# Performance work log

Hardware: AMD Instinct MI355X
Metric: run time of the kernel (lower is better)

## Reference

```python
import jax, jax.numpy as jnp
import numpy as np

B, N, D, H = 8, 2048, 256, 4
HD = D // H


def setup_inputs() -> dict:
    key = jax.random.key(0)
    ks = jax.random.split(key, 12)
    s = 1.0 / np.sqrt(D)
    inp = {
        "node_features": jax.random.normal(ks[0], (B, N, D), dtype=jnp.float32),
        "causal_mask": jnp.tril(jnp.ones((N, N), dtype=jnp.float32)),
        "Wq": jax.random.normal(ks[1], (D, D), dtype=jnp.float32) * s,
        "bq": jnp.zeros((D,), dtype=jnp.float32),
        "Wk": jax.random.normal(ks[2], (D, D), dtype=jnp.float32) * s,
        "bk": jnp.zeros((D,), dtype=jnp.float32),
        "Wv": jax.random.normal(ks[3], (D, D), dtype=jnp.float32) * s,
        "bv": jnp.zeros((D,), dtype=jnp.float32),
        "Wo": jax.random.normal(ks[4], (D, D), dtype=jnp.float32) * s,
        "bo": jnp.zeros((D,), dtype=jnp.float32),
        "Wu": jax.random.normal(ks[5], (2 * D, D), dtype=jnp.float32) * (1.0 / np.sqrt(2 * D)),
        "bu": jnp.zeros((D,), dtype=jnp.float32),
    }
    return inp


def reference(node_features, causal_mask, Wq, bq, Wk, bk, Wv, bv, Wo, bo, Wu, bu):
    # node_features: [B, N, D]; causal_mask: [N, N] (1 = keep, 0 = masked)
    x = node_features
    # project and split heads -> [B, H, N, HD]
    def heads(w, b):
        return (x @ w + b).reshape(B, N, H, HD).transpose(0, 2, 1, 3)
    q, k, v = heads(Wq, bq), heads(Wk, bk), heads(Wv, bv)
    scale = 1.0 / np.sqrt(HD).astype(np.float32)
    scores = jnp.einsum("bhnd,bhmd->bhnm", q, k) * scale  # [B, H, N, N]
    scores = jnp.where(causal_mask > 0, scores, jnp.float32(-1e9))
    attn = jax.nn.softmax(scores, axis=-1)
    ctx = jnp.einsum("bhnm,bhmd->bhnd", attn, v)  # [B, H, N, HD]
    messages = ctx.transpose(0, 2, 1, 3).reshape(B, N, D) @ Wo + bo  # [B, N, D]
    combined = jnp.concatenate([x, messages], axis=-1)  # [B, N, 2D]
    updated = jax.nn.relu(combined @ Wu + bu)  # [B, N, D]  (dropout = identity in eval)
    return updated
```

## Files before the change

kernel.cpp:

```cpp
#include <hip/hip_runtime.h>
#include <math.h>

constexpr int B  = 8;
constexpr int N  = 2048;
constexpr int D  = 256;
constexpr int H  = 4;
constexpr int HD = 64;
constexpr int MTOT = B * N;

typedef __attribute__((ext_vector_type(8))) short  short8;
typedef __attribute__((ext_vector_type(4))) float  floatx4;
typedef unsigned short ushort_t;

#define QSCALE 0.1803368801111204f

__device__ __forceinline__ unsigned short f2bf(float f) {
    unsigned u = __float_as_uint(f);
    u += 0x7fffu + ((u >> 16) & 1u);
    return (unsigned short)(u >> 16);
}

__device__ __forceinline__ unsigned short f2bf_t(float f) {
    return (unsigned short)(__float_as_uint(f) >> 16);
}

__device__ __forceinline__ void gl_lds16(const ushort_t* g, ushort_t* l) {
    __builtin_amdgcn_global_load_lds(
        (const __attribute__((address_space(1))) void*)g,
        (__attribute__((address_space(3))) void*)l, 16, 0, 0);
}

__global__ __launch_bounds__(256) void prep(
    const float* __restrict__ x,
    const float* __restrict__ Wq, const float* __restrict__ Wk,
    const float* __restrict__ Wv, const float* __restrict__ Wo,
    const float* __restrict__ Wu,
    ushort_t* __restrict__ xb,
    ushort_t* __restrict__ wqkvt, ushort_t* __restrict__ wut,
    ushort_t* __restrict__ wbt,   ushort_t* __restrict__ wob)
{
    __shared__ float Ls[64][65];
    const int bx = blockIdx.x;
    const int t  = threadIdx.x;

    if (bx < 2048) {
        int idx = (bx * 256 + t) * 8;
        float4 a = *(const float4*)(x + idx);
        float4 b = *(const float4*)(x + idx + 4);
        ushort_t o[8] = {f2bf(a.x), f2bf(a.y), f2bf(a.z), f2bf(a.w),
                         f2bf(b.x), f2bf(b.y), f2bf(b.z), f2bf(b.w)};
        *(short8*)(xb + idx) = *(const short8*)o;
        return;
    }

    if (bx < 2112) {
        const int e  = bx - 2048;
        const int zz = e >> 4;
        const int kt = (e >> 2) & 3;
        const int nt = e & 3;
        const float* src; ushort_t* dst; int K;
        if      (zz == 0) { src = Wq; dst = wqkvt;          K = 256; }
        else if (zz == 1) { src = Wk; dst = wqkvt + 65536;  K = 256; }
        else if (zz == 2) { src = Wv; dst = wqkvt + 131072; K = 256; }
        else              { src = Wu; dst = wut;            K = 512; }
        #pragma unroll
        for (int i = 0; i < 16; i++) {
            int ee = t + i * 256, r = ee >> 6, c = ee & 63;
            Ls[r][c] = src[(size_t)(kt * 64 + r) * 256 + nt * 64 + c];
        }
        __syncthreads();
        #pragma unroll
        for (int i = 0; i < 16; i++) {
            int ee = t + i * 256, r = ee >> 6, c = ee & 63;
            dst[(size_t)(nt * 64 + r) * K + kt * 64 + c] = f2bf(Ls[c][r]);
        }
        return;
    }

    if (bx < 2128) {
        const int e  = bx - 2112;
        const int kt = e >> 2;
        const int nt = e & 3;
        #pragma unroll
        for (int i = 0; i < 16; i++) {
            int ee = t + i * 256, r = ee >> 6, c = ee & 63;
            Ls[r][c] = Wu[(size_t)(256 + kt * 64 + r) * 256 + nt * 64 + c];
        }
        __syncthreads();
        #pragma unroll
        for (int i = 0; i < 16; i++) {
            int ee = t + i * 256, r = ee >> 6, c = ee & 63;
            wbt[(size_t)(nt * 64 + r) * 256 + kt * 64 + c] = f2bf(Ls[c][r]);
        }
        return;
    }

    {
        int idx = ((bx - 2128) * 256 + t) * 8;
        float4 a = *(const float4*)(Wo + idx);
        float4 b = *(const float4*)(Wo + idx + 4);
        ushort_t o[8] = {f2bf(a.x), f2bf(a.y), f2bf(a.z), f2bf(a.w),
                         f2bf(b.x), f2bf(b.y), f2bf(b.z), f2bf(b.w)};
        *(short8*)(wob + idx) = *(const short8*)o;
    }
}

__global__ __launch_bounds__(256) void qkv_gemm(
    const ushort_t* __restrict__ xb, const ushort_t* __restrict__ wqkvt,
    const ushort_t* __restrict__ wob, const ushort_t* __restrict__ wbt,
    const float* __restrict__ Wu,
    const float* __restrict__ bq, const float* __restrict__ bk,
    const float* __restrict__ bv, const float* __restrict__ bo,
    const float* __restrict__ bu,
    ushort_t* __restrict__ q, ushort_t* __restrict__ kout,
    ushort_t* __restrict__ vt,
    ushort_t* __restrict__ wut, float* __restrict__ b2)
{
    __shared__ ushort_t SH[16896];
    ushort_t* As = SH;
    ushort_t* Bs = SH + 8192;

    const int t = threadIdx.x, w = t >> 6, lane = t & 63;
    const int quad = lane >> 4, l16 = lane & 15;
    const int bx = blockIdx.x;
    const int wr = (w >> 1) * 64, wc = (w & 1) * 64;

    if (blockIdx.y == 128) {
        if (bx < 4) {
            const int row0 = (bx >> 1) * 128;
            const int col0 = (bx & 1) * 128;
            floatx4 acc[4][4] = {};
            for (int k0 = 0; k0 < 256; k0 += 64) {
                __syncthreads();
                #pragma unroll
                for (int i = 0; i < 4; i++) {
                    int e = t + (i << 8);
                    int r = e >> 3, c8 = (e & 7) << 3;
                    gl_lds16(wob + (size_t)(row0 + r) * 256 + k0 + c8, &As[e * 8]);
                    gl_lds16(wbt + (size_t)(col0 + r) * 256 + k0 + c8, &Bs[e * 8]);
                }
                __syncthreads();
                #pragma unroll
                for (int kk = 0; kk < 64; kk += 32) {
                    short8 af[4], bf[4];
                    #pragma unroll
                    for (int i = 0; i < 4; i++)
                        af[i] = *(const short8*)&As[(wr + i * 16 + l16) * 64 + kk + quad * 8];
                    #pragma unroll
                    for (int j = 0; j < 4; j++)
                        bf[j] = *(const short8*)&Bs[(wc + j * 16 + l16) * 64 + kk + quad * 8];
                    #pragma unroll
                    for (int i = 0; i < 4; i++)
                        #pragma unroll
                        for (int j = 0; j < 4; j++)
                            acc[i][j] = __builtin_amdgcn_mfma_f32_16x16x32_bf16(
                                af[i], bf[j], acc[i][j], 0, 0, 0);
                }
            }
            #pragma unroll
            for (int j = 0; j < 4; j++) {
                int cl = wc + j * 16 + l16;
                #pragma unroll
                for (int i = 0; i < 4; i++)
                    #pragma unroll
                    for (int r = 0; r < 4; r++) {
                        int ml = wr + i * 16 + quad * 4 + r;
                        wut[(size_t)(col0 + cl) * 512 + 256 + row0 + ml] =
                            f2bf(acc[i][j][r]);
                    }
            }
        } else if (bx == 4) {
            float s0 = 0.f, s1 = 0.f, s2 = 0.f, s3 = 0.f;
            for (int j = 0; j < 64; j++) {
                s0 = fmaf(bo[j],       Wu[(size_t)(256 + j)       * 256 + t], s0);
                s1 = fmaf(bo[j + 64],  Wu[(size_t)(256 + j + 64)  * 256 + t], s1);
                s2 = fmaf(bo[j + 128], Wu[(size_t)(256 + j + 128) * 256 + t], s2);
                s3 = fmaf(bo[j + 192], Wu[(size_t)(256 + j + 192) * 256 + t], s3);
            }
            b2[t] = bu[t] + ((s0 + s1) + (s2 + s3));
        }
        return;
    }

    const int col0 = bx * 128, row0 = blockIdx.y * 128;

    floatx4 acc[4][4] = {};

    for (int k0 = 0; k0 < 256; k0 += 64) {
        __syncthreads();
        #pragma unroll
        for (int i = 0; i < 4; i++) {
            int e = t + (i << 8);
            int r = e >> 3, c8 = (e & 7) << 3;
            gl_lds16(xb    + (size_t)(row0 + r) * 256 + k0 + c8, &As[e * 8]);
            gl_lds16(wqkvt + (size_t)(col0 + r) * 256 + k0 + c8, &Bs[e * 8]);
        }
        __syncthreads();

        #pragma unroll
        for (int kk = 0; kk < 64; kk += 32) {
            short8 af[4], bf[4];
            #pragma unroll
            for (int i = 0; i < 4; i++)
                af[i] = *(const short8*)&As[(wr + i * 16 + l16) * 64 + kk + quad * 8];
            #pragma unroll
            for (int j = 0; j < 4; j++)
                bf[j] = *(const short8*)&Bs[(wc + j * 16 + l16) * 64 + kk + quad * 8];
            #pragma unroll
            for (int i = 0; i < 4; i++)
                #pragma unroll
                for (int j = 0; j < 4; j++)
                    acc[i][j] = __builtin_amdgcn_mfma_f32_16x16x32_bf16(
                        af[i], bf[j], acc[i][j], 0, 0, 0);
        }
    }

    const int kind = bx >> 1;
    const float* bias = (kind == 0) ? bq : (kind == 1 ? bk : bv);
    const float scl  = (kind == 0) ? QSCALE : 1.0f;
    __syncthreads();
    ushort_t (*Ts)[132] = (ushort_t(*)[132])SH;
    #pragma unroll
    for (int j = 0; j < 4; j++) {
        int cl = wc + j * 16 + l16;
        float bsv = bias[(bx & 1) * 128 + cl];
        #pragma unroll
        for (int i = 0; i < 4; i++) {
            #pragma unroll
            for (int r = 0; r < 4; r++) {
                int ml = wr + i * 16 + quad * 4 + r;
                ushort_t bvv = f2bf((acc[i][j][r] + bsv) * scl);
                if (kind < 2) Ts[ml][cl] = bvv;
                else          Ts[cl][ml] = bvv;
            }
        }
    }
    __syncthreads();

    const int b = row0 >> 11, n0 = row0 & (N - 1);
    #pragma unroll
    for (int i = 0; i < 8; i++) {
        int id = t + (i << 8);
        int rr = id >> 4, c8 = (id & 15) << 3;
        short8 val = *(const short8*)&Ts[rr][c8];
        if (kind < 2) {
            int cg = (bx & 1) * 128 + c8;
            int h = cg >> 6, hd = cg & 63;
            if (kind == 0) {
                *(short8*)&q[(((size_t)(b * H + h)) * N + n0 + rr) * HD + hd] = val;
            } else {
                int hd2 = (((hd >> 3) ^ (rr & 7)) << 3);
                *(short8*)&kout[(((size_t)(b * H + h)) * N + n0 + rr) * HD + hd2] = val;
            }
        } else {
            int cg = (bx & 1) * 128 + rr;
            int h = cg >> 6, hd = cg & 63;
            int u  = id & 15;
            int up = (u & 8) | ((u ^ hd) & 7);
            *(short8*)&vt[(((size_t)(b * H + h)) * HD + hd) * N + n0 + (up << 3)] = val;
        }
    }
}

__global__ __launch_bounds__(512) void attn_mfma(
    const ushort_t* __restrict__ q,
    const ushort_t* __restrict__ k,
    const ushort_t* __restrict__ vt,
    ushort_t* __restrict__ ctxb)
{
    __shared__ ushort_t Ks [128 * 64];
    __shared__ ushort_t Vts[64 * 128];
    __shared__ ushort_t Ps [8][16][36];

    const int t    = threadIdx.x;
    const int w    = t >> 6;
    const int lane = t & 63;
    const int quad = lane >> 4;
    const int l16  = lane & 15;
    const int swz  = l16 & 7;
    const int bh   = blockIdx.x;
    const int b    = bh >> 2, h = bh & 3;
    const int by   = blockIdx.y;
    const int grp  = w >> 2;
    const int qt   = grp ? by : (31 - by);
    const int qbase = qt * 64;
    const int rowb  = qbase + (w & 3) * 16;

    const ushort_t* qp = q  + (size_t)bh * N * HD;
    const ushort_t* kp = k  + (size_t)bh * N * HD;
    const ushort_t* vp = vt + (size_t)bh * HD * N;

    short8 qf0, qf1;
    {
        const ushort_t* qrow = qp + (size_t)(rowb + l16) * HD + quad * 8;
        qf0 = *(const short8*)(qrow);
        qf1 = *(const short8*)(qrow + 32);
    }

    floatx4 acc_o[4] = {};
    float plsum[4] = {};

    const int nkt_self = (qt >> 1) + 1;
    const int nkt_max  = ((31 - by) >> 1) + 1;

    for (int kt = 0; kt < nkt_max; kt++) {
        const int kbase = kt * 128;
        __syncthreads();

        #pragma unroll
        for (int i = 0; i < 2; i++) {
            int e = t + (i << 9);
            gl_lds16(kp + (((size_t)(kbase + (e >> 3))) << 6) + ((e & 7) << 3),
                     &Ks[e * 8]);
            gl_lds16(vp + (size_t)(e >> 4) * N + kbase + ((e & 15) << 3),
                     &Vts[e * 8]);
        }
        __syncthreads();

        if (kt >= nkt_self) continue;

        int rem = rowb + 15 - kbase;
        int nch = (rem < 0) ? 0 : ((rem >> 5) + 1);
        if (nch > 4) nch = 4;

        for (int ch = 0; ch < nch; ch++) {
            #pragma unroll
            for (int c2 = 0; c2 < 2; c2++) {
                const int ct = ch * 2 + c2;
                const int krow = (ct * 16 + l16) * 64;
                short8 kf0 = *(const short8*)&Ks[krow + ((quad ^ swz) << 3)];
                short8 kf1 = *(const short8*)&Ks[krow + (((4 + quad) ^ swz) << 3)];
                floatx4 z = {0.0f, 0.0f, 0.0f, 0.0f};
                floatx4 s = __builtin_amdgcn_mfma_f32_16x16x32_bf16(qf0, kf0, z, 0, 0, 0);
                s         = __builtin_amdgcn_mfma_f32_16x16x32_bf16(qf1, kf1, s, 0, 0, 0);
                const bool partial = (kbase + ct * 16 + 15) > rowb;
                if (partial) {
                    const int keyg = kbase + ct * 16 + l16;
                    #pragma unroll
                    for (int r = 0; r < 4; r++) {
                        float sv = s[r];
                        if (keyg > rowb + quad * 4 + r) sv = -3.0e38f;
                        float pv = __builtin_amdgcn_exp2f(sv);
                        plsum[r] += pv;
                        Ps[w][quad * 4 + r][c2 * 16 + l16] = f2bf_t(pv);
                    }
                } else {
                    #pragma unroll
                    for (int r = 0; r < 4; r++) {
                        float pv = __builtin_amdgcn_exp2f(s[r]);
                        plsum[r] += pv;
                        Ps[w][quad * 4 + r][c2 * 16 + l16] = f2bf_t(pv);
                    }
                }
            }
            short8 pf = *(const short8*)&Ps[w][l16][quad * 8];
            const int uu = ch * 4 + quad;
            const int up = (uu & 8) | ((uu ^ l16) & 7);
            #pragma unroll
            for (int nt = 0; nt < 4; nt++) {
                short8 vf = *(const short8*)&Vts[(nt * 16 + l16) * 128 + (up << 3)];
                acc_o[nt] = __builtin_amdgcn_mfma_f32_16x16x32_bf16(pf, vf, acc_o[nt], 0, 0, 0);
            }
        }
    }

    #pragma unroll
    for (int r = 0; r < 4; r++) {
        float l = plsum[r];
        l += __shfl_xor(l, 1);
        l += __shfl_xor(l, 2);
        l += __shfl_xor(l, 4);
        l += __shfl_xor(l, 8);
        float inv = 1.0f / l;
        int   n   = rowb + quad * 4 + r;
        #pragma unroll
        for (int nt = 0; nt < 4; nt++) {
            ctxb[((size_t)(b * N + n)) * D + h * HD + nt * 16 + l16] =
                f2bf(acc_o[nt][r] * inv);
        }
    }
}

__global__ __launch_bounds__(256) void tail2(
    const ushort_t* __restrict__ xb, const ushort_t* __restrict__ ctxb,
    const ushort_t* __restrict__ wut, const float* __restrict__ b2,
    float* __restrict__ out)
{
    __shared__ ushort_t As[64 * 64];
    __shared__ ushort_t Bs[128 * 64];

    const int t = threadIdx.x, w = t >> 6, lane = t & 63;
    const int quad = lane >> 4, l16 = lane & 15;
    const int col0 = blockIdx.x * 128, row0 = blockIdx.y * 64;
    const int wr = (w >> 1) * 32, wc = (w & 1) * 64;

    floatx4 acc[2][4] = {};

    for (int k0 = 0; k0 < 512; k0 += 64) {
        const ushort_t* Ab = (k0 < 256) ? xb : ctxb;
        const int ka = k0 & 255;
        __syncthreads();
        #pragma unroll
        for (int i = 0; i < 2; i++) {
            int e = t + (i << 8);
            int r = e >> 3, c8 = (e & 7) << 3;
            gl_lds16(Ab + (size_t)(row0 + r) * 256 + ka + c8, &As[e * 8]);
        }
        #pragma unroll
        for (int i = 0; i < 4; i++) {
            int e = t + (i << 8);
            int r = e >> 3, c8 = (e & 7) << 3;
            gl_lds16(wut + (size_t)(col0 + r) * 512 + k0 + c8, &Bs[e * 8]);
        }
        __syncthreads();

        #pragma unroll
        for (int kk = 0; kk < 64; kk += 32) {
            short8 af[2], bf[4];
            #pragma unroll
            for (int i = 0; i < 2; i++)
                af[i] = *(const short8*)&As[(wr + i * 16 + l16) * 64 + kk + quad * 8];
            #pragma unroll
            for (int j = 0; j < 4; j++)
                bf[j] = *(const short8*)&Bs[(wc + j * 16 + l16) * 64 + kk + quad * 8];
            #pragma unroll
            for (int i = 0; i < 2; i++)
                #pragma unroll
                for (int j = 0; j < 4; j++)
                    acc[i][j] = __builtin_amdgcn_mfma_f32_16x16x32_bf16(
                        af[i], bf[j], acc[i][j], 0, 0, 0);
        }
    }

    #pragma unroll
    for (int j = 0; j < 4; j++) {
        int col = col0 + wc + j * 16 + l16;
        float bsv = b2[col];
        #pragma unroll
        for (int i = 0; i < 2; i++) {
            #pragma unroll
            for (int r = 0; r < 4; r++) {
                int m = row0 + wr + i * 16 + quad * 4 + r;
                out[(size_t)m * 256 + col] = fmaxf(acc[i][j][r] + bsv, 0.0f);
            }
        }
    }
}

extern "C" void kernel_launch(void* const* d_in, const int* in_sizes, int n_in,
                              void* d_out, int out_size, void* d_ws, size_t ws_size,
                              hipStream_t stream)
{
    const float* x  = (const float*)d_in[0];
    const float* Wq = (const float*)d_in[2];
    const float* bq = (const float*)d_in[3];
    const float* Wk = (const float*)d_in[4];
    const float* bk = (const float*)d_in[5];
    const float* Wv = (const float*)d_in[6];
    const float* bv = (const float*)d_in[7];
    const float* Wo = (const float*)d_in[8];
    const float* bo = (const float*)d_in[9];
    const float* Wu = (const float*)d_in[10];
    const float* bu = (const float*)d_in[11];
    float* out = (float*)d_out;

    const size_t SZ = (size_t)MTOT * D;
    ushort_t* xb    = (ushort_t*)d_ws;
    ushort_t* qb    = xb    + SZ;
    ushort_t* kb    = qb    + SZ;
    ushort_t* vbt   = kb    + SZ;
    ushort_t* ctxb  = vbt   + SZ;
    ushort_t* wqkvt = ctxb  + SZ;
    ushort_t* wut   = wqkvt + 196608;
    ushort_t* wbt   = wut   + 131072;
    ushort_t* wob   = wbt   + 65536;
    float*    b2    = (float*)(wob + 65536);

    prep<<<2160, 256, 0, stream>>>(x, Wq, Wk, Wv, Wo, Wu,
                                   xb, wqkvt, wut, wbt, wob);

    qkv_gemm<<<dim3(6, 129), 256, 0, stream>>>(
        xb, wqkvt, wob, wbt, Wu, bq, bk, bv, bo, bu,
        qb, kb, vbt, wut, b2);

    attn_mfma<<<dim3(32, 16), 512, 0, stream>>>(qb, kb, vbt, ctxb);

    tail2<<<dim3(2, 256), 256, 0, stream>>>(xb, ctxb, wut, b2, out);
}
```

Measured before the change: 171.6 us.

## Double-buffer LDS tiles in QKV and tail GEMMs to overlap loads with MFMA

Both the QKV projection GEMM and the tail output GEMM now prefetch the next K-slice into a second LDS buffer while MFMAs run on the current one, replacing the load-sync-compute-sync loop with a single barrier per step. The QKV kernel shrinks its K-step to 32 so two buffers fit in the existing shared array, and it folds the W2 side-GEMM path into the same pipelined loop. The goal is to hide global-to-LDS latency. In exchange the tail kernel doubles its LDS footprint, which may reduce occupancy, and the QKV loop now has more iterations.

```diff
diff --git a/kernel.cpp b/kernel.cpp
--- a/kernel.cpp
+++ b/kernel.cpp
@@ -117,59 +117,15 @@
     ushort_t* __restrict__ wut, float* __restrict__ b2)
 {
     __shared__ ushort_t SH[16896];
-    ushort_t* As = SH;
-    ushort_t* Bs = SH + 8192;
 
     const int t = threadIdx.x, w = t >> 6, lane = t & 63;
     const int quad = lane >> 4, l16 = lane & 15;
     const int bx = blockIdx.x;
     const int wr = (w >> 1) * 64, wc = (w & 1) * 64;
-
-    if (blockIdx.y == 128) {
-        if (bx < 4) {
-            const int row0 = (bx >> 1) * 128;
-            const int col0 = (bx & 1) * 128;
-            floatx4 acc[4][4] = {};
-            for (int k0 = 0; k0 < 256; k0 += 64) {
-                __syncthreads();
-                #pragma unroll
-                for (int i = 0; i < 4; i++) {
-                    int e = t + (i << 8);
-                    int r = e >> 3, c8 = (e & 7) << 3;
-                    gl_lds16(wob + (size_t)(row0 + r) * 256 + k0 + c8, &As[e * 8]);
-                    gl_lds16(wbt + (size_t)(col0 + r) * 256 + k0 + c8, &Bs[e * 8]);
-                }
-                __syncthreads();
-                #pragma unroll
-                for (int kk = 0; kk < 64; kk += 32) {
-                    short8 af[4], bf[4];
-                    #pragma unroll
-                    for (int i = 0; i < 4; i++)
-                        af[i] = *(const short8*)&As[(wr + i * 16 + l16) * 64 + kk + quad * 8];
-                    #pragma unroll
-                    for (int j = 0; j < 4; j++)
-                        bf[j] = *(const short8*)&Bs[(wc + j * 16 + l16) * 64 + kk + quad * 8];
-                    #pragma unroll
-                    for (int i = 0; i < 4; i++)
-                        #pragma unroll
-                        for (int j = 0; j < 4; j++)
-                            acc[i][j] = __builtin_amdgcn_mfma_f32_16x16x32_bf16(
-                                af[i], bf[j], acc[i][j], 0, 0, 0);
-                }
-            }
-            #pragma unroll
-            for (int j = 0; j < 4; j++) {
-                int cl = wc + j * 16 + l16;
-                #pragma unroll
-                for (int i = 0; i < 4; i++)
-                    #pragma unroll
-                    for (int r = 0; r < 4; r++) {
-                        int ml = wr + i * 16 + quad * 4 + r;
-                        wut[(size_t)(col0 + cl) * 512 + 256 + row0 + ml] =
-                            f2bf(acc[i][j][r]);
-                    }
-            }
-        } else if (bx == 4) {
+    const bool isW2 = (blockIdx.y == 128);
+
+    if (isW2 && bx >= 4) {
+        if (bx == 4) {
             float s0 = 0.f, s1 = 0.f, s2 = 0.f, s3 = 0.f;
             for (int j = 0; j < 64; j++) {
                 s0 = fmaf(bo[j],       Wu[(size_t)(256 + j)       * 256 + t], s0);
@@ -182,43 +138,74 @@
         return;
     }
 
-    const int col0 = bx * 128, row0 = blockIdx.y * 128;
+    const int row0 = isW2 ? ((bx >> 1) * 128) : ((int)blockIdx.y * 128);
+    const int col0 = isW2 ? ((bx & 1) * 128) : (bx * 128);
+    const ushort_t* Ag = (isW2 ? wob : xb)    + (size_t)row0 * 256;
+    const ushort_t* Bg = (isW2 ? wbt : wqkvt) + (size_t)col0 * 256;
 
     floatx4 acc[4][4] = {};
 
-    for (int k0 = 0; k0 < 256; k0 += 64) {
-        __syncthreads();
-        #pragma unroll
-        for (int i = 0; i < 4; i++) {
+    {
+        #pragma unroll
+        for (int i = 0; i < 2; i++) {
             int e = t + (i << 8);
-            int r = e >> 3, c8 = (e & 7) << 3;
-            gl_lds16(xb    + (size_t)(row0 + r) * 256 + k0 + c8, &As[e * 8]);
-            gl_lds16(wqkvt + (size_t)(col0 + r) * 256 + k0 + c8, &Bs[e * 8]);
-        }
-        __syncthreads();
-
-        #pragma unroll
-        for (int kk = 0; kk < 64; kk += 32) {
-            short8 af[4], bf[4];
-            #pragma unroll
-            for (int i = 0; i < 4; i++)
-                af[i] = *(const short8*)&As[(wr + i * 16 + l16) * 64 + kk + quad * 8];
+            int r = e >> 2, c8 = (e & 3) << 3;
+            gl_lds16(Ag + (size_t)r * 256 + c8, SH + e * 8);
+            gl_lds16(Bg + (size_t)r * 256 + c8, SH + 8192 + e * 8);
+        }
+    }
+    __syncthreads();
+
+    for (int k = 0; k < 8; k++) {
+        const int buf = k & 1;
+        if (k < 7) {
+            const int nb = buf ^ 1;
+            const int k0 = (k + 1) * 32;
+            #pragma unroll
+            for (int i = 0; i < 2; i++) {
+                int e = t + (i << 8);
+                int r = e >> 2, c8 = (e & 3) << 3;
+                gl_lds16(Ag + (size_t)r * 256 + k0 + c8, SH + nb * 4096 + e * 8);
+                gl_lds16(Bg + (size_t)r * 256 + k0 + c8, SH + 8192 + nb * 4096 + e * 8);
+            }
+        }
+        const ushort_t* Al = SH + buf * 4096;
+        const ushort_t* Bl = SH + 8192 + buf * 4096;
+        short8 af[4], bf[4];
+        #pragma unroll
+        for (int i = 0; i < 4; i++)
+            af[i] = *(const short8*)&Al[(wr + i * 16 + l16) * 32 + quad * 8];
+        #pragma unroll
+        for (int j = 0; j < 4; j++)
+            bf[j] = *(const short8*)&Bl[(wc + j * 16 + l16) * 32 + quad * 8];
+        #pragma unroll
+        for (int i = 0; i < 4; i++)
             #pragma unroll
             for (int j = 0; j < 4; j++)
-                bf[j] = *(const short8*)&Bs[(wc + j * 16 + l16) * 64 + kk + quad * 8];
+                acc[i][j] = __builtin_amdgcn_mfma_f32_16x16x32_bf16(
+                    af[i], bf[j], acc[i][j], 0, 0, 0);
+        __syncthreads();
+    }
+
+    if (isW2) {
+        #pragma unroll
+        for (int j = 0; j < 4; j++) {
+            int cl = wc + j * 16 + l16;
             #pragma unroll
             for (int i = 0; i < 4; i++)
                 #pragma unroll
-                for (int j = 0; j < 4; j++)
-                    acc[i][j] = __builtin_amdgcn_mfma_f32_16x16x32_bf16(
-                        af[i], bf[j], acc[i][j], 0, 0, 0);
-        }
+                for (int r = 0; r < 4; r++) {
+                    int ml = wr + i * 16 + quad * 4 + r;
+                    wut[(size_t)(col0 + cl) * 512 + 256 + row0 + ml] =
+                        f2bf(acc[i][j][r]);
+                }
+        }
+        return;
     }
 
     const int kind = bx >> 1;
     const float* bias = (kind == 0) ? bq : (kind == 1 ? bk : bv);
     const float scl  = (kind == 0) ? QSCALE : 1.0f;
-    __syncthreads();
     ushort_t (*Ts)[132] = (ushort_t(*)[132])SH;
     #pragma unroll
     for (int j = 0; j < 4; j++) {
@@ -386,8 +373,8 @@
     const ushort_t* __restrict__ wut, const float* __restrict__ b2,
     float* __restrict__ out)
 {
-    __shared__ ushort_t As[64 * 64];
-    __shared__ ushort_t Bs[128 * 64];
+    __shared__ ushort_t As2[2][64 * 64];
+    __shared__ ushort_t Bs2[2][128 * 64];
 
     const int t = threadIdx.x, w = t >> 6, lane = t & 63;
     const int quad = lane >> 4, l16 = lane & 15;
@@ -396,33 +383,51 @@
 
     floatx4 acc[2][4] = {};
 
-    for (int k0 = 0; k0 < 512; k0 += 64) {
-        const ushort_t* Ab = (k0 < 256) ? xb : ctxb;
-        const int ka = k0 & 255;
-        __syncthreads();
+    {
         #pragma unroll
         for (int i = 0; i < 2; i++) {
             int e = t + (i << 8);
             int r = e >> 3, c8 = (e & 7) << 3;
-            gl_lds16(Ab + (size_t)(row0 + r) * 256 + ka + c8, &As[e * 8]);
+            gl_lds16(xb + (size_t)(row0 + r) * 256 + c8, &As2[0][e * 8]);
         }
         #pragma unroll
         for (int i = 0; i < 4; i++) {
             int e = t + (i << 8);
             int r = e >> 3, c8 = (e & 7) << 3;
-            gl_lds16(wut + (size_t)(col0 + r) * 512 + k0 + c8, &Bs[e * 8]);
-        }
-        __syncthreads();
-
+            gl_lds16(wut + (size_t)(col0 + r) * 512 + c8, &Bs2[0][e * 8]);
+        }
+    }
+    __syncthreads();
+
+    for (int k = 0; k < 8; k++) {
+        const int buf = k & 1;
+        if (k < 7) {
+            const int nb = buf ^ 1;
+            const int kn = k + 1;
+            const ushort_t* Ab = (kn < 4) ? xb : ctxb;
+            const int ka = (kn & 3) * 64;
+            #pragma unroll
+            for (int i = 0; i < 2; i++) {
+                int e = t + (i << 8);
+                int r = e >> 3, c8 = (e & 7) << 3;
+                gl_lds16(Ab + (size_t)(row0 + r) * 256 + ka + c8, &As2[nb][e * 8]);
+            }
+            #pragma unroll
+            for (int i = 0; i < 4; i++) {
+                int e = t + (i << 8);
+                int r = e >> 3, c8 = (e & 7) << 3;
+                gl_lds16(wut + (size_t)(col0 + r) * 512 + kn * 64 + c8, &Bs2[nb][e * 8]);
+            }
+        }
         #pragma unroll
         for (int kk = 0; kk < 64; kk += 32) {
             short8 af[2], bf[4];
             #pragma unroll
             for (int i = 0; i < 2; i++)
-                af[i] = *(const short8*)&As[(wr + i * 16 + l16) * 64 + kk + quad * 8];
+                af[i] = *(const short8*)&As2[buf][(wr + i * 16 + l16) * 64 + kk + quad * 8];
             #pragma unroll
             for (int j = 0; j < 4; j++)
-                bf[j] = *(const short8*)&Bs[(wc + j * 16 + l16) * 64 + kk + quad * 8];
+                bf[j] = *(const short8*)&Bs2[buf][(wc + j * 16 + l16) * 64 + kk + quad * 8];
             #pragma unroll
             for (int i = 0; i < 2; i++)
                 #pragma unroll
@@ -430,6 +435,7 @@
                     acc[i][j] = __builtin_amdgcn_mfma_f32_16x16x32_bf16(
                         af[i], bf[j], acc[i][j], 0, 0, 0);
         }
+        __syncthreads();
     }
 
     #pragma unroll
```

New measurement: 175.7 us. 2.4% more time.
